# Kernel optimization log

Measured on AMD Instinct MI355X. Metric: run time of the kernel, lower is better.

Reference implementation:

```python
import jax, jax.numpy as jnp
import numpy as np

B, H, HKV, S, D = 2, 16, 4, 4096, 64
BN = 64            # block size (BLOCK_N)
G = 64             # num_global_tokens (== one block)
NB = S // BN       # total kv blocks
WINDOW = 3         # local window blocks per query block
NRAND = 3          # random blocks per query block
BPQ = WINDOW + NRAND
SCALE = 1.0 / float(np.sqrt(D))
NEG = -1e30


def setup_inputs() -> dict:
    key = jax.random.key(0)
    kq, kk, kv = jax.random.split(key, 3)
    q = jax.random.normal(kq, (B, H, S, D), jnp.float32)
    k = jax.random.normal(kk, (B, HKV, S, D), jnp.float32)
    v = jax.random.normal(kv, (B, HKV, S, D), jnp.float32)
    # 4 contiguous segments per batch row
    seg = jnp.arange(S, dtype=jnp.int32) // (S // 4)
    segment_ids = jnp.broadcast_to(seg, (B, S))
    alibi_slopes = jnp.asarray(2.0 ** (-8.0 * np.arange(1, H + 1) / H), jnp.float32)
    # block indices: per query block, window blocks + random blocks; -1 = skip
    rng = np.random.default_rng(0)
    bi = np.full((NB, BPQ), -1, np.int64)
    first = G // BN  # first sparse query block (global block handled separately)
    for i in range(first, NB):
        win = [b if first <= b < NB else -1 for b in (i - 1, i, i + 1)]
        rnd = rng.integers(first, NB, size=NRAND).tolist()
        bi[i] = win + rnd
    block_indices = jnp.asarray(bi)
    return {"q": q, "k": k, "v": v, "segment_ids": segment_ids,
            "block_indices": block_indices, "alibi_slopes": alibi_slopes}


def _softmax_attend(scores, values):
    m = jnp.max(scores, axis=-1, keepdims=True)
    p = jnp.exp(scores - m)
    l = jnp.sum(p, axis=-1, keepdims=True)
    l = jnp.where(l == 0.0, 1.0, l)
    return jnp.einsum('...qk,...kd->...qd', p / l, values)


def _forward(q, k, v, alibi_slopes, segment_ids, block_indices):
    hpg = H // HKV
    kf = jnp.repeat(k, hpg, axis=1)  # [B,H,S,D]
    vf = jnp.repeat(v, hpg, axis=1)
    pos = jnp.arange(S, dtype=jnp.float32)
    seg = segment_ids

    # ---- global queries: first G tokens attend to the full sequence ----
    qg = q[:, :, :G]
    sc_g = jnp.einsum('bhgd,bhsd->bhgs', qg, kf) * SCALE
    bias_g = -alibi_slopes[None, :, None, None] * jnp.abs(
        pos[:G][None, None, :, None] - pos[None, None, None, :])
    sc_g = sc_g + bias_g
    same_g = (seg[:, :G, None] == seg[:, None, :]) & (seg[:, :G, None] >= 0)
    sc_g = jnp.where(same_g[:, None], sc_g, NEG)
    out_g = _softmax_attend(sc_g, vf)  # [B,H,G,D]

    # ---- sparse query blocks: global KV + gathered window/random blocks ----
    first = G // BN
    nq = NB - first
    K = BPQ * BN
    qs = q[:, :, G:].reshape(B, H, nq, BN, D)
    bi = block_indices[first:]                      # [nq,BPQ]
    bi_safe = jnp.where(bi >= 0, bi, 0)
    kb = kf.reshape(B, H, NB, BN, D)[:, :, bi_safe].reshape(B, H, nq, K, D)
    vb = vf.reshape(B, H, NB, BN, D)[:, :, bi_safe].reshape(B, H, nq, K, D)
    kposi = (bi_safe * BN)[:, :, None] + jnp.arange(BN)      # [nq,BPQ,BN]
    valid = (jnp.broadcast_to((bi >= 0)[:, :, None], kposi.shape)
             & (kposi < S) & (kposi >= G)).reshape(nq, K)
    kposi = kposi.reshape(nq, K)
    kposf = kposi.astype(jnp.float32)
    qpos = jnp.arange(G, S, dtype=jnp.float32).reshape(nq, BN)
    qseg = seg[:, G:].reshape(B, nq, BN)
    kseg = seg[:, kposi]                            # [B,nq,K]

    sc_b = jnp.einsum('bhqmd,bhqnd->bhqmn', qs, kb) * SCALE
    sc_b = sc_b - alibi_slopes[None, :, None, None, None] * jnp.abs(
        qpos[:, :, None] - kposf[:, None, :])[None, None]
    same_b = (qseg[:, :, :, None] == kseg[:, :, None, :]) & (qseg[:, :, :, None] >= 0)
    sc_b = jnp.where((same_b & valid[None, :, None, :])[:, None], sc_b, NEG)

    gk, gv = kf[:, :, :G], vf[:, :, :G]
    sc_gk = jnp.einsum('bhqmd,bhgd->bhqmg', qs, gk) * SCALE
    sc_gk = sc_gk - alibi_slopes[None, :, None, None, None] * jnp.abs(
        qpos[:, :, None] - pos[:G][None, None, :])[None, None]
    gseg = seg[:, :G]
    same_gk = (qseg[:, :, :, None] == gseg[:, None, None, :]) & (qseg[:, :, :, None] >= 0)
    sc_gk = jnp.where(same_gk[:, None], sc_gk, NEG)

    scores = jnp.concatenate([sc_gk, sc_b], axis=-1)         # [B,H,nq,BN,G+K]
    vals = jnp.concatenate(
        [jnp.broadcast_to(gv[:, :, None], (B, H, nq, G, D)), vb], axis=-2)
    out_s = _softmax_attend(scores, vals).reshape(B, H, S - G, D)

    return jnp.concatenate([out_g, out_s], axis=2)           # [B,H,S,D]


def reference(q, k, v, segment_ids, block_indices, alibi_slopes):
    return _forward(q, k, v, alibi_slopes, segment_ids, block_indices)
```

## Files before the change

### kernel.cpp

```cpp
#include <hip/hip_runtime.h>
#include <hip/hip_bf16.h>

#define B_ 2
#define H_ 16
#define HKV_ 4
#define HPG_ 4
#define S_ 4096
#define D_ 64
#define BN_ 64
#define NB_ 64
#define BPQ_ 6
#define QSCALE_LOG2 0.18033688f
#define LOG2E 1.44269504f
#define LDK 72
#define NSPLIT0 4
#define PART2_ 16896

typedef short bf16x8 __attribute__((ext_vector_type(8)));
typedef short bf16x4v __attribute__((ext_vector_type(4)));
typedef float f32x4 __attribute__((ext_vector_type(4)));
typedef unsigned int u32x4 __attribute__((ext_vector_type(4)));

static __device__ __forceinline__ short f2bf(float f) {
    unsigned u = __builtin_bit_cast(unsigned, f);
    unsigned r = u + 0x7FFFu + ((u >> 16) & 1u);
    return (short)(r >> 16);
}

static __device__ __forceinline__ unsigned cvt_pk_bf16(float lo, float hi) {
    unsigned r;
    asm("v_cvt_pk_bf16_f32 %0, %1, %2" : "=v"(r) : "v"(lo), "v"(hi));
    return r;
}

__global__ __launch_bounds__(512, 2) void sparse_attn_main(
    const float* __restrict__ q,
    const float* __restrict__ k,
    const float* __restrict__ v,
    const int* __restrict__ seg,
    const int* __restrict__ bidx,
    const float* __restrict__ slopes,
    float* __restrict__ out,
    float* __restrict__ ws)
{
    __shared__ __align__(16) short kc[2][BN_ * LDK];
    __shared__ __align__(16) short vt[2][BN_ * LDK];
    __shared__ int vlist[17];
    __shared__ int vcount;

    const int qbx  = blockIdx.x;
    int qb, split;
    if (qbx < NB_) { qb = qbx; split = 0; }
    else           { qb = 0;   split = qbx - (NB_ - 1); }
    const bool split_path = (qb == 0);

    const int y    = blockIdx.y;
    const int b    = y / HKV_;
    const int hkv  = y % HKV_;
    const int tid  = threadIdx.x;
    const int wave = tid >> 6;
    const int g    = wave >> 1;
    const int half = wave & 1;
    const int lane = tid & 63;
    const int l16  = lane & 15;
    const int lhi  = lane >> 4;
    const int h    = hkv * HPG_ + g;

    const float slope2 = slopes[h] * LOG2E;
    const int   qseg   = seg[b * S_ + qb * BN_];

    if (wave == 0) {
        const int n = split_path ? 16 : (1 + BPQ_);
        int cand = -1;
        if (lane < n) {
            if (split_path)       cand = split + 4 * lane;
            else if (lane == 0)   cand = 0;
            else                  cand = bidx[qb * BPQ_ + lane - 1];
        }
        bool ok = false;
        if (cand >= 0 && cand < NB_) {
            int ks_ = seg[b * S_ + cand * BN_];
            ok = (qseg >= 0) && (ks_ == qseg);
        }
        unsigned long long m = __ballot(ok);
        if (ok) {
            int rank = __popcll(m & ((1ull << lane) - 1ull));
            vlist[rank] = cand;
        }
        if (lane == 0) vcount = (int)__popcll(m);
    }

    bf16x8 qf[2][2];
    float qpos[2];
#pragma unroll
    for (int j = 0; j < 2; ++j) {
        const int qrow = qb * BN_ + half * 32 + j * 16 + l16;
        qpos[j] = (float)qrow;
        const float* qp = q + (((size_t)(b * H_ + h)) * S_ + qrow) * D_;
#pragma unroll
        for (int kk = 0; kk < 2; ++kk)
#pragma unroll
            for (int i = 0; i < 8; ++i)
                qf[j][kk][i] = f2bf(qp[kk * 32 + lhi * 8 + i] * QSCALE_LOG2);
    }

    f32x4 oacc[2][4] = {};
    float mrun[2] = { -1e30f, -1e30f }, lrun[2] = { 0.f, 0.f };

    const float* kb_ptr = k + ((size_t)(b * HKV_ + hkv)) * S_ * D_;
    const float* vb_ptr = v + ((size_t)(b * HKV_ + hkv)) * S_ * D_;

    float4 kr0, kr1, vr0, vr1;
#define ISSUE_LOADS(CBLK) do { \
        const float4* ks_ = (const float4*)(kb_ptr + (size_t)(CBLK) * (BN_ * D_)); \
        const float4* vs_ = (const float4*)(vb_ptr + (size_t)(CBLK) * (BN_ * D_)); \
        kr0 = ks_[tid];       kr1 = ks_[tid + 512]; \
        vr0 = vs_[tid];       vr1 = vs_[tid + 512]; \
    } while (0)

#define WST1(P, IDX, KR, VR) do { \
        int key_ = (IDX) >> 4; \
        int d0_  = ((IDX) & 15) * 4; \
        uint2 kp_ = { cvt_pk_bf16(KR.x, KR.y), cvt_pk_bf16(KR.z, KR.w) }; \
        *(uint2*)&kc[P][key_ * LDK + d0_] = kp_; \
        int sw_ = key_ ^ (((d0_ >> 2) & 7) << 3); \
        vt[P][(d0_ + 0) * LDK + sw_] = f2bf(VR.x); \
        vt[P][(d0_ + 1) * LDK + sw_] = f2bf(VR.y); \
        vt[P][(d0_ + 2) * LDK + sw_] = f2bf(VR.z); \
        vt[P][(d0_ + 3) * LDK + sw_] = f2bf(VR.w); \
    } while (0)
#define WRITE_STAGE(P) do { WST1(P, tid, kr0, vr0); WST1(P, tid + 512, kr1, vr1); } while (0)

    __syncthreads();
    const int nval = vcount;

    ISSUE_LOADS(vlist[0]);
    WRITE_STAGE(0);
    if (nval > 1) ISSUE_LOADS(vlist[1]);
    __syncthreads();

    for (int c = 0; c < nval; ++c) {
        const int p = c & 1;
        const int kbase = vlist[c] * BN_;

        if (c + 1 < nval) {
            WRITE_STAGE(p ^ 1);
            if (c + 2 < nval) ISSUE_LOADS(vlist[c + 2]);
        }

        f32x4 sacc[2][4] = {};
#pragma unroll
        for (int nt = 0; nt < 4; ++nt)
#pragma unroll
            for (int kk = 0; kk < 2; ++kk) {
                bf16x8 kf_ = *(const bf16x8*)&kc[p][(nt * 16 + l16) * LDK + kk * 32 + lhi * 8];
                sacc[0][nt] = __builtin_amdgcn_mfma_f32_16x16x32_bf16(kf_, qf[0][kk], sacc[0][nt], 0, 0, 0);
                sacc[1][nt] = __builtin_amdgcn_mfma_f32_16x16x32_bf16(kf_, qf[1][kk], sacc[1][nt], 0, 0, 0);
            }

        unsigned pk_[2][4][2];
#pragma unroll
        for (int j = 0; j < 2; ++j) {
            const float dbase = qpos[j] - (float)(kbase + lhi * 4);
            float mx = -1e30f;
#pragma unroll
            for (int nt = 0; nt < 4; ++nt)
#pragma unroll
                for (int r2 = 0; r2 < 4; ++r2) {
                    float sc = fmaf(-slope2, fabsf(dbase - (float)(nt * 16 + r2)), sacc[j][nt][r2]);
                    sacc[j][nt][r2] = sc;
                    mx = fmaxf(mx, sc);
                }
            mx = fmaxf(mx, __shfl_xor(mx, 16));
            mx = fmaxf(mx, __shfl_xor(mx, 32));
            const float mn = fmaxf(mrun[j], mx);
            float sum = 0.f;
#pragma unroll
            for (int nt = 0; nt < 4; ++nt) {
                float p0 = exp2f(sacc[j][nt][0] - mn);
                float p1 = exp2f(sacc[j][nt][1] - mn);
                float p2 = exp2f(sacc[j][nt][2] - mn);
                float p3 = exp2f(sacc[j][nt][3] - mn);
                sum += (p0 + p1) + (p2 + p3);
                pk_[j][nt][0] = cvt_pk_bf16(p0, p1);
                pk_[j][nt][1] = cvt_pk_bf16(p2, p3);
            }
            sum += __shfl_xor(sum, 16);
            sum += __shfl_xor(sum, 32);
            const float corr = exp2f(mrun[j] - mn);
            mrun[j] = mn;
            lrun[j] = lrun[j] * corr + sum;
#pragma unroll
            for (int dt = 0; dt < 4; ++dt) oacc[j][dt] *= corr;
        }

#pragma unroll
        for (int kk = 0; kk < 2; ++kk) {
            bf16x8 pf[2];
#pragma unroll
            for (int j = 0; j < 2; ++j) {
                u32x4 pw = { pk_[j][2 * kk][0], pk_[j][2 * kk][1],
                             pk_[j][2 * kk + 1][0], pk_[j][2 * kk + 1][1] };
                pf[j] = __builtin_bit_cast(bf16x8, pw);
            }
#pragma unroll
            for (int dt = 0; dt < 4; ++dt) {
                const short* vrow = &vt[p][(dt * 16 + l16) * LDK];
                const int sv8 = ((4 * dt + (l16 >> 2)) & 7) << 3;
                bf16x4v lo = *(const bf16x4v*)&vrow[(kk * 32 + 4 * lhi) ^ sv8];
                bf16x4v hi = *(const bf16x4v*)&vrow[(kk * 32 + 16 + 4 * lhi) ^ sv8];
                bf16x8 vf = __builtin_shufflevector(lo, hi, 0, 1, 2, 3, 4, 5, 6, 7);
                oacc[0][dt] = __builtin_amdgcn_mfma_f32_16x16x32_bf16(vf, pf[0], oacc[0][dt], 0, 0, 0);
                oacc[1][dt] = __builtin_amdgcn_mfma_f32_16x16x32_bf16(vf, pf[1], oacc[1][dt], 0, 0, 0);
            }
        }

        __syncthreads();
    }

    if (split_path) {
        float* wsp = ws + (size_t)((b * HKV_ + hkv) * NSPLIT0 + split) * PART2_;
#pragma unroll
        for (int j = 0; j < 2; ++j) {
            const int row = half * 32 + j * 16 + l16;
#pragma unroll
            for (int dt = 0; dt < 4; ++dt) {
                float4 o4 = { oacc[j][dt][0], oacc[j][dt][1], oacc[j][dt][2], oacc[j][dt][3] };
                *(float4*)&wsp[g * 4096 + row * 64 + dt * 16 + 4 * lhi] = o4;
            }
            if (lhi == 0) {
                wsp[16384 + g * 64 + row] = mrun[j];
                wsp[16640 + g * 64 + row] = lrun[j];
            }
        }
    } else {
#pragma unroll
        for (int j = 0; j < 2; ++j) {
            const float inv = 1.0f / (lrun[j] == 0.f ? 1.f : lrun[j]);
            float* op = out + (((size_t)(b * H_ + h)) * S_ + qb * BN_ + half * 32 + j * 16 + l16) * D_;
#pragma unroll
            for (int dt = 0; dt < 4; ++dt) {
                float4 o4 = { oacc[j][dt][0] * inv, oacc[j][dt][1] * inv,
                              oacc[j][dt][2] * inv, oacc[j][dt][3] * inv };
                *(float4*)&op[dt * 16 + 4 * lhi] = o4;
            }
        }
    }
}

__global__ __launch_bounds__(256) void sparse_attn_combine(
    const float* __restrict__ ws,
    float* __restrict__ out)
{
    const int bh  = blockIdx.x;
    const int b   = bh / H_;
    const int h   = bh % H_;
    const int hkv = h >> 2;
    const int g   = h & 3;
    const int t   = threadIdx.x;
    const int row = t >> 2;
    const int d0  = (t & 3) * 16;

    const float* base = ws + (size_t)(b * HKV_ + hkv) * NSPLIT0 * PART2_;
    float ms[NSPLIT0], ls[NSPLIT0];
    float M = -1e30f;
#pragma unroll
    for (int s = 0; s < NSPLIT0; ++s) {
        ms[s] = base[s * PART2_ + 16384 + g * 64 + row];
        ls[s] = base[s * PART2_ + 16640 + g * 64 + row];
        M = fmaxf(M, ms[s]);
    }
    float w[NSPLIT0];
    float L = 0.f;
#pragma unroll
    for (int s = 0; s < NSPLIT0; ++s) {
        w[s] = exp2f(ms[s] - M);
        L += w[s] * ls[s];
    }
    const float inv = 1.0f / (L == 0.f ? 1.f : L);

    float* op = out + ((size_t)bh * S_ + row) * D_ + d0;
#pragma unroll
    for (int jj = 0; jj < 16; ++jj) {
        float acc = 0.f;
#pragma unroll
        for (int s = 0; s < NSPLIT0; ++s)
            acc += w[s] * base[s * PART2_ + g * 4096 + row * 64 + d0 + jj];
        op[jj] = acc * inv;
    }
}

extern "C" void kernel_launch(void* const* d_in, const int* in_sizes, int n_in,
                              void* d_out, int out_size, void* d_ws, size_t ws_size,
                              hipStream_t stream) {
    const float* q      = (const float*)d_in[0];
    const float* k      = (const float*)d_in[1];
    const float* v      = (const float*)d_in[2];
    const int*   seg    = (const int*)d_in[3];
    const int*   bidx   = (const int*)d_in[4];
    const float* slopes = (const float*)d_in[5];
    float*       out    = (float*)d_out;
    float*       ws     = (float*)d_ws;

    dim3 grid(NB_ + (NSPLIT0 - 1), B_ * HKV_);
    sparse_attn_main<<<grid, 512, 0, stream>>>(q, k, v, seg, bidx, slopes, out, ws);
    sparse_attn_combine<<<dim3(B_ * H_), 256, 0, stream>>>(ws, out);
}
```

Before: 140.0 us.

## Process two KV blocks per barrier with a four-slot LDS ring

Grows the K/V shared-memory staging from two buffers to four and processes two KV blocks per loop iteration, with one __syncthreads per pair instead of one per block. Global loads and LDS writes for the next pair are interleaved with the compute of the current pair. This targets barrier overhead and aims to give loads more time in flight. The cost is doubled LDS use, from about 36 KB to about 72 KB per block, which together with __launch_bounds__(512,2) may cut occupancy. The extra unrolled compute may also add register pressure.

```diff
diff --git a/kernel.cpp b/kernel.cpp
--- a/kernel.cpp
+++ b/kernel.cpp
@@ -43,8 +43,8 @@
     float* __restrict__ out,
     float* __restrict__ ws)
 {
-    __shared__ __align__(16) short kc[2][BN_ * LDK];
-    __shared__ __align__(16) short vt[2][BN_ * LDK];
+    __shared__ __align__(16) short kc[4][BN_ * LDK];
+    __shared__ __align__(16) short vt[4][BN_ * LDK];
     __shared__ int vlist[17];
     __shared__ int vcount;
 
@@ -131,89 +131,98 @@
     } while (0)
 #define WRITE_STAGE(P) do { WST1(P, tid, kr0, vr0); WST1(P, tid + 512, kr1, vr1); } while (0)
 
+#define COMPUTE(SLOT, KBASE) do { \
+        f32x4 sacc[2][4] = {}; \
+        _Pragma("unroll") \
+        for (int nt = 0; nt < 4; ++nt) \
+            _Pragma("unroll") \
+            for (int kk = 0; kk < 2; ++kk) { \
+                bf16x8 kf_ = *(const bf16x8*)&kc[SLOT][(nt * 16 + l16) * LDK + kk * 32 + lhi * 8]; \
+                sacc[0][nt] = __builtin_amdgcn_mfma_f32_16x16x32_bf16(kf_, qf[0][kk], sacc[0][nt], 0, 0, 0); \
+                sacc[1][nt] = __builtin_amdgcn_mfma_f32_16x16x32_bf16(kf_, qf[1][kk], sacc[1][nt], 0, 0, 0); \
+            } \
+        unsigned pk_[2][4][2]; \
+        _Pragma("unroll") \
+        for (int j = 0; j < 2; ++j) { \
+            const float dbase = qpos[j] - (float)((KBASE) + lhi * 4); \
+            float mx = -1e30f; \
+            _Pragma("unroll") \
+            for (int nt = 0; nt < 4; ++nt) \
+                _Pragma("unroll") \
+                for (int r2 = 0; r2 < 4; ++r2) { \
+                    float sc = fmaf(-slope2, fabsf(dbase - (float)(nt * 16 + r2)), sacc[j][nt][r2]); \
+                    sacc[j][nt][r2] = sc; \
+                    mx = fmaxf(mx, sc); \
+                } \
+            mx = fmaxf(mx, __shfl_xor(mx, 16)); \
+            mx = fmaxf(mx, __shfl_xor(mx, 32)); \
+            const float mn = fmaxf(mrun[j], mx); \
+            float sum = 0.f; \
+            _Pragma("unroll") \
+            for (int nt = 0; nt < 4; ++nt) { \
+                float p0 = exp2f(sacc[j][nt][0] - mn); \
+                float p1 = exp2f(sacc[j][nt][1] - mn); \
+                float p2 = exp2f(sacc[j][nt][2] - mn); \
+                float p3 = exp2f(sacc[j][nt][3] - mn); \
+                sum += (p0 + p1) + (p2 + p3); \
+                pk_[j][nt][0] = cvt_pk_bf16(p0, p1); \
+                pk_[j][nt][1] = cvt_pk_bf16(p2, p3); \
+            } \
+            sum += __shfl_xor(sum, 16); \
+            sum += __shfl_xor(sum, 32); \
+            const float corr = exp2f(mrun[j] - mn); \
+            mrun[j] = mn; \
+            lrun[j] = lrun[j] * corr + sum; \
+            _Pragma("unroll") \
+            for (int dt = 0; dt < 4; ++dt) oacc[j][dt] *= corr; \
+        } \
+        _Pragma("unroll") \
+        for (int kk = 0; kk < 2; ++kk) { \
+            bf16x8 pf[2]; \
+            _Pragma("unroll") \
+            for (int j = 0; j < 2; ++j) { \
+                u32x4 pw = { pk_[j][2 * kk][0], pk_[j][2 * kk][1], \
+                             pk_[j][2 * kk + 1][0], pk_[j][2 * kk + 1][1] }; \
+                pf[j] = __builtin_bit_cast(bf16x8, pw); \
+            } \
+            _Pragma("unroll") \
+            for (int dt = 0; dt < 4; ++dt) { \
+                const short* vrow = &vt[SLOT][(dt * 16 + l16) * LDK]; \
+                const int sv8 = ((4 * dt + (l16 >> 2)) & 7) << 3; \
+                bf16x4v lo = *(const bf16x4v*)&vrow[(kk * 32 + 4 * lhi) ^ sv8]; \
+                bf16x4v hi = *(const bf16x4v*)&vrow[(kk * 32 + 16 + 4 * lhi) ^ sv8]; \
+                bf16x8 vf = __builtin_shufflevector(lo, hi, 0, 1, 2, 3, 4, 5, 6, 7); \
+                oacc[0][dt] = __builtin_amdgcn_mfma_f32_16x16x32_bf16(vf, pf[0], oacc[0][dt], 0, 0, 0); \
+                oacc[1][dt] = __builtin_amdgcn_mfma_f32_16x16x32_bf16(vf, pf[1], oacc[1][dt], 0, 0, 0); \
+            } \
+        } \
+    } while (0)
+
     __syncthreads();
     const int nval = vcount;
 
     ISSUE_LOADS(vlist[0]);
     WRITE_STAGE(0);
-    if (nval > 1) ISSUE_LOADS(vlist[1]);
+    if (nval > 1) { ISSUE_LOADS(vlist[1]); WRITE_STAGE(1); }
+    if (nval > 2) ISSUE_LOADS(vlist[2]);
     __syncthreads();
 
-    for (int c = 0; c < nval; ++c) {
-        const int p = c & 1;
-        const int kbase = vlist[c] * BN_;
-
-        if (c + 1 < nval) {
-            WRITE_STAGE(p ^ 1);
-            if (c + 2 < nval) ISSUE_LOADS(vlist[c + 2]);
-        }
-
-        f32x4 sacc[2][4] = {};
-#pragma unroll
-        for (int nt = 0; nt < 4; ++nt)
-#pragma unroll
-            for (int kk = 0; kk < 2; ++kk) {
-                bf16x8 kf_ = *(const bf16x8*)&kc[p][(nt * 16 + l16) * LDK + kk * 32 + lhi * 8];
-                sacc[0][nt] = __builtin_amdgcn_mfma_f32_16x16x32_bf16(kf_, qf[0][kk], sacc[0][nt], 0, 0, 0);
-                sacc[1][nt] = __builtin_amdgcn_mfma_f32_16x16x32_bf16(kf_, qf[1][kk], sacc[1][nt], 0, 0, 0);
-            }
-
-        unsigned pk_[2][4][2];
-#pragma unroll
-        for (int j = 0; j < 2; ++j) {
-            const float dbase = qpos[j] - (float)(kbase + lhi * 4);
-            float mx = -1e30f;
-#pragma unroll
-            for (int nt = 0; nt < 4; ++nt)
-#pragma unroll
-                for (int r2 = 0; r2 < 4; ++r2) {
-                    float sc = fmaf(-slope2, fabsf(dbase - (float)(nt * 16 + r2)), sacc[j][nt][r2]);
-                    sacc[j][nt][r2] = sc;
-                    mx = fmaxf(mx, sc);
-                }
-            mx = fmaxf(mx, __shfl_xor(mx, 16));
-            mx = fmaxf(mx, __shfl_xor(mx, 32));
-            const float mn = fmaxf(mrun[j], mx);
-            float sum = 0.f;
-#pragma unroll
-            for (int nt = 0; nt < 4; ++nt) {
-                float p0 = exp2f(sacc[j][nt][0] - mn);
-                float p1 = exp2f(sacc[j][nt][1] - mn);
-                float p2 = exp2f(sacc[j][nt][2] - mn);
-                float p3 = exp2f(sacc[j][nt][3] - mn);
-                sum += (p0 + p1) + (p2 + p3);
-                pk_[j][nt][0] = cvt_pk_bf16(p0, p1);
-                pk_[j][nt][1] = cvt_pk_bf16(p2, p3);
-            }
-            sum += __shfl_xor(sum, 16);
-            sum += __shfl_xor(sum, 32);
-            const float corr = exp2f(mrun[j] - mn);
-            mrun[j] = mn;
-            lrun[j] = lrun[j] * corr + sum;
-#pragma unroll
-            for (int dt = 0; dt < 4; ++dt) oacc[j][dt] *= corr;
-        }
-
-#pragma unroll
-        for (int kk = 0; kk < 2; ++kk) {
-            bf16x8 pf[2];
-#pragma unroll
-            for (int j = 0; j < 2; ++j) {
-                u32x4 pw = { pk_[j][2 * kk][0], pk_[j][2 * kk][1],
-                             pk_[j][2 * kk + 1][0], pk_[j][2 * kk + 1][1] };
-                pf[j] = __builtin_bit_cast(bf16x8, pw);
-            }
-#pragma unroll
-            for (int dt = 0; dt < 4; ++dt) {
-                const short* vrow = &vt[p][(dt * 16 + l16) * LDK];
-                const int sv8 = ((4 * dt + (l16 >> 2)) & 7) << 3;
-                bf16x4v lo = *(const bf16x4v*)&vrow[(kk * 32 + 4 * lhi) ^ sv8];
-                bf16x4v hi = *(const bf16x4v*)&vrow[(kk * 32 + 16 + 4 * lhi) ^ sv8];
-                bf16x8 vf = __builtin_shufflevector(lo, hi, 0, 1, 2, 3, 4, 5, 6, 7);
-                oacc[0][dt] = __builtin_amdgcn_mfma_f32_16x16x32_bf16(vf, pf[0], oacc[0][dt], 0, 0, 0);
-                oacc[1][dt] = __builtin_amdgcn_mfma_f32_16x16x32_bf16(vf, pf[1], oacc[1][dt], 0, 0, 0);
-            }
-        }
+    const int nr = (nval + 1) >> 1;
+    for (int r = 0; r < nr; ++r) {
+        const int p  = r & 1;
+        const int s0 = 2 * p, s1 = 2 * p + 1;
+        const int t0 = 2 * (p ^ 1), t1 = 2 * (p ^ 1) + 1;
+        const int c0 = 2 * r, c1 = 2 * r + 1;
+
+        if (c0 + 2 < nval) WRITE_STAGE(t0);
+        if (c0 + 3 < nval) ISSUE_LOADS(vlist[c0 + 3]);
+
+        COMPUTE(s0, vlist[c0] * BN_);
+
+        if (c0 + 3 < nval) WRITE_STAGE(t1);
+        if (c0 + 4 < nval) ISSUE_LOADS(vlist[c0 + 4]);
+
+        if (c1 < nval) COMPUTE(s1, vlist[c1] * BN_);
 
         __syncthreads();
     }
```

Result: no change. 140.2 us (+0.1%).
